# Kernel optimization log

Hardware: AMD Instinct MI355X
Metric: run time of the kernel (lower is better)

## Reference

```python
import jax, jax.numpy as jnp
import numpy as np
import math

PH, PW = 14, 14      # patch size
DH, DW = 3, 3        # DCT block size
BINS = 256


def _dct_matrix(size: int) -> np.ndarray:
    m = np.zeros((size, size), dtype=np.float32)
    for i in range(size):
        for j in range(size):
            if i == 0:
                m[i, j] = math.sqrt(1.0 / size)
            else:
                m[i, j] = math.sqrt(2.0 / size) * math.cos(math.pi * (2 * j + 1) * i / (2 * size))
    return m


def setup_inputs() -> dict:
    key = jax.random.key(0)
    x = jax.random.uniform(key, (16, 3, 448, 448), dtype=jnp.float32)
    dct_matrix = jnp.asarray(_dct_matrix(DH))
    return {"x": x, "dct_matrix": dct_matrix}


def reference(x, dct_matrix):
    B, C, H, W = x.shape
    Hp, Wp = H // PH, W // PW
    # extract non-overlapping patches -> (B, Hp, Wp, C, PH, PW)
    patches = x.reshape(B, C, Hp, PH, Wp, PW).transpose(0, 2, 4, 1, 3, 5)

    # ---- per-patch pixel-value entropy (histogram via scatter-add) ----
    N = PH * PW
    pi = jnp.clip(jnp.round(jax.lax.stop_gradient(patches) * 255.0), 0, 255).astype(jnp.int32)
    flat = pi.reshape(-1, N)                       # (P, N), P = B*Hp*Wp*C
    P = flat.shape[0]
    counts = jnp.zeros((P, BINS), jnp.float32).at[jnp.arange(P)[:, None], flat].add(1.0)
    prob = counts / N + 1e-10
    entropy = -(prob * jnp.log2(prob)).sum(-1).reshape(B, Hp, Wp, C)

    # ---- sliding 3x3 windows inside each patch (stride 1) ----
    n = PH - DH + 1                                # 12 window positions per axis
    wins = jnp.stack(
        [patches[..., di:di + n, dj:dj + n] for di in range(DH) for dj in range(DW)],
        axis=-1,
    ).reshape(B, Hp, Wp, C, n, n, DH, DW)          # last two dims = within-window offsets

    # 2D DCT: D @ block @ D^T
    dct = jnp.einsum('ij,...jk,lk->...il', dct_matrix, wins, dct_matrix)

    # ---- direction variance of normalized stds ----
    S1 = jnp.std(dct, axis=-1).mean(-1)                       # rows
    S2 = jnp.std(dct, axis=-2).mean(-1)                       # cols
    S3 = jnp.std(jnp.diagonal(dct, axis1=-2, axis2=-1), axis=-1)
    S4 = jnp.std(jnp.diagonal(jnp.flip(dct, axis=-1), axis1=-2, axis2=-1), axis=-1)
    S = (S1 + S2 + S3 + S4) / 4.0 + 1e-8
    psi = jnp.var(jnp.stack([S1 / S, S2 / S, S3 / S, S4 / S], axis=-1), axis=-1, ddof=1)
    psi_m = psi.mean(axis=(-1, -2))                           # (B, Hp, Wp, C)

    richness = psi_m * entropy
    return richness.mean(-1)                                  # (B, Hp, Wp)
```

## Files before the change

### kernel.cpp

```cpp
#include <hip/hip_runtime.h>
#include <math.h>


typedef unsigned int uint32;

__device__ __forceinline__ float fsqrt_fast(float x) { return __builtin_amdgcn_sqrtf(x); }
__device__ __forceinline__ float frcp_fast(float x)  { return __builtin_amdgcn_rcpf(x);  }
__device__ __forceinline__ float flog2_fast(float x) { return __builtin_amdgcn_logf(x);  }

__device__ __forceinline__ float std3_fast(float a, float b, float c) {
    float s = a + b + c;
    float q = fmaf(a, a, fmaf(b, b, c * c));
    float v = fmaf(q, (1.0f / 3.0f), (s * s) * (-1.0f / 9.0f));
    return fsqrt_fast(fmaxf(v, 0.0f));
}

struct RunData {
    float2 a0, a1, a2, a3, b0, b1, b2, b3, c0, c1, c2, c3;
};

__device__ __forceinline__ RunData load_run(const float* base) {
    RunData r;
    r.a0 = *reinterpret_cast<const float2*>(base + 0);
    r.a1 = *reinterpret_cast<const float2*>(base + 2);
    r.a2 = *reinterpret_cast<const float2*>(base + 4);
    r.a3 = *reinterpret_cast<const float2*>(base + 6);
    r.b0 = *reinterpret_cast<const float2*>(base + 448);
    r.b1 = *reinterpret_cast<const float2*>(base + 450);
    r.b2 = *reinterpret_cast<const float2*>(base + 452);
    r.b3 = *reinterpret_cast<const float2*>(base + 454);
    r.c0 = *reinterpret_cast<const float2*>(base + 896);
    r.c1 = *reinterpret_cast<const float2*>(base + 898);
    r.c2 = *reinterpret_cast<const float2*>(base + 900);
    r.c3 = *reinterpret_cast<const float2*>(base + 902);
    return r;
}

__device__ __forceinline__ float run_psi(const RunData& rd, float k0, float k1, float k2) {
    float r0[8] = { rd.a0.x, rd.a0.y, rd.a1.x, rd.a1.y, rd.a2.x, rd.a2.y, rd.a3.x, rd.a3.y };
    float r1[8] = { rd.b0.x, rd.b0.y, rd.b1.x, rd.b1.y, rd.b2.x, rd.b2.y, rd.b3.x, rd.b3.y };
    float r2[8] = { rd.c0.x, rd.c0.y, rd.c1.x, rd.c1.y, rd.c2.x, rd.c2.y, rd.c3.x, rd.c3.y };

    float t0[8], t1[8], t2[8];
#pragma unroll
    for (int J = 0; J < 8; ++J) {
        float s = r0[J] + r2[J];
        t0[J] = k0 * (s + r1[J]);
        t1[J] = k1 * (r0[J] - r2[J]);
        t2[J] = k2 * fmaf(-2.0f, r1[J], s);
    }

    float psi_run = 0.0f;
#pragma unroll
    for (int m = 0; m < 6; ++m) {
        float X0 = t0[m],     X1 = t1[m],     X2 = t2[m];
        float Y0 = t0[m + 1], Y1 = t1[m + 1], Y2 = t2[m + 1];
        float Z0 = t0[m + 2], Z1 = t1[m + 2], Z2 = t2[m + 2];
        float xz0 = X0 + Z0, xz1 = X1 + Z1, xz2 = X2 + Z2;
        float d00 = k0 * (xz0 + Y0), d01 = k1 * (X0 - Z0), d02 = k2 * fmaf(-2.0f, Y0, xz0);
        float d10 = k0 * (xz1 + Y1), d11 = k1 * (X1 - Z1), d12 = k2 * fmaf(-2.0f, Y1, xz1);
        float d20 = k0 * (xz2 + Y2), d21 = k1 * (X2 - Z2), d22 = k2 * fmaf(-2.0f, Y2, xz2);

        float S1 = (std3_fast(d00, d01, d02) + std3_fast(d10, d11, d12) + std3_fast(d20, d21, d22)) * (1.0f / 3.0f);
        float S2 = (std3_fast(d00, d10, d20) + std3_fast(d01, d11, d21) + std3_fast(d02, d12, d22)) * (1.0f / 3.0f);
        float S3 = std3_fast(d00, d11, d22);
        float S4 = std3_fast(d02, d11, d20);

        float sumS = (S1 + S2) + (S3 + S4);
        float sumQ = fmaf(S1, S1, fmaf(S2, S2, fmaf(S3, S3, S4 * S4)));
        float h    = fmaxf(fmaf(-0.25f * sumS, sumS, sumQ), 0.0f);
        float Sm   = fmaf(sumS, 0.25f, 1e-8f);
        float inv  = frcp_fast(Sm);
        psi_run    = fmaf(h * inv * inv, (1.0f / 3.0f), psi_run);
    }
    return psi_run;
}

#define BIN4_1CH(V, COL) { \
        _Pragma("unroll") \
        for (int e_ = 0; e_ < 4; ++e_) { \
            float val_ = (&(V).x)[e_]; \
            int bin_ = (int)rintf(val_ * 255.0f);    \
            bin_ = min(max(bin_, 0), 255); \
            int ce_ = (COL) + e_; \
            int p_  = (ce_ * 2341) >> 15;            \
            atomicAdd(&hist[p_ >> 2][bin_], 1u << ((p_ & 3) * 8)); \
        }}

__global__ __launch_bounds__(192, 8) void rich_pc_kernel(
    const float* __restrict__ x,
    const float* __restrict__ dctm,
    float* __restrict__ ws)
{
    const int bid = blockIdx.x;
    const int ch  = bid >> 11;
    const int r_  = bid & 2047;
    const int wpg = r_ & 3;
    const int hp  = (r_ >> 2) & 31;
    const int b   = r_ >> 7;
    const int tid = threadIdx.x;

    __shared__ uint32 hist[2][256];
    __shared__ float  psiPart[8][24];
    __shared__ float  entAcc[8];

    const float k0 = dctm[0];
    const float k1 = dctm[3];
    const float k2 = dctm[6];

    for (int i = tid; i < 512; i += 192) ((uint32*)hist)[i] = 0u;
    __syncthreads();

    const size_t plane = ((size_t)(b * 3 + ch) * 448 + hp * 14) * 448 + wpg * 112;

    const int pl   = tid / 24;
    const int rr   = tid - pl * 24;
    const int wi   = rr >> 1, half = rr & 1;
    const float* base = x + plane + (size_t)wi * 448 + pl * 14 + half * 6;

    int row0 = tid / 28,  col0 = (tid - row0 * 28) * 4;
    int t1_  = tid + 192;
    int row1 = t1_ / 28,  col1 = (t1_ - row1 * 28) * 4;
    const float* src0 = x + plane + (size_t)row0 * 448 + col0;
    const float* src1 = x + plane + (size_t)row1 * 448 + col1;

    RunData rd = load_run(base);
    float4 h0 = *reinterpret_cast<const float4*>(src0);
    float4 h1 = *reinterpret_cast<const float4*>(src1);

    float psi = run_psi(rd, k0, k1, k2);
    psiPart[pl][rr] = psi;

    BIN4_1CH(h0, col0)
    BIN4_1CH(h1, col1)
    if (tid < 8) {
        int colT = (20 + tid) * 4;
        const float* srcT = x + plane + (size_t)13 * 448 + colT;
        float4 hT = *reinterpret_cast<const float4*>(srcT);
        BIN4_1CH(hT, colT)
    }
    __syncthreads();

    if (tid < 64) {
        const int pcE = tid >> 3, sub = tid & 7;
        const int rowW = pcE >> 2, sh = (pcE & 3) * 8;
        float negent = 0.0f;
#pragma unroll
        for (int kk = 0; kk < 32; ++kk) {
            uint32 c = (hist[rowW][sub + 8 * kk] >> sh) & 0xffu;
            float pr = (float)c * (1.0f / 196.0f) + 1e-10f;
            negent = fmaf(pr, flog2_fast(pr), negent);
        }
#pragma unroll
        for (int off = 1; off < 8; off <<= 1) negent += __shfl_xor(negent, off, 64);
        if (sub == 0) entAcc[pcE] = -negent;
    }
    __syncthreads();

    if (tid < 8) {
        float s = 0.0f;
#pragma unroll
        for (int r = 0; r < 24; ++r) s += psiPart[tid][r];
        ws[ch * 16384 + ((b * 32 + hp) * 32 + wpg * 8 + tid)] =
            (s * (1.0f / 144.0f)) * entAcc[tid];
    }
}

__global__ __launch_bounds__(256) void combine_kernel(
    const float* __restrict__ ws, float* __restrict__ out)
{
    int i = blockIdx.x * 256 + threadIdx.x;
    out[i] = (ws[i] + ws[16384 + i] + ws[32768 + i]) * (1.0f / 3.0f);
}

__global__ __launch_bounds__(192, 6) void richness_kernel(
    const float* __restrict__ x,
    const float* __restrict__ dctm,
    float* __restrict__ out)
{
    const int bid = blockIdx.x;
    const int wpg = bid & 3;
    const int hp  = (bid >> 2) & 31;
    const int b   = bid >> 7;
    const int tid = threadIdx.x;

    __shared__ uint32 hist[6][256];
    __shared__ float  psiPart[24][24];
    __shared__ float  entAcc[24];
    __shared__ float  richAcc[24];

    const float k0 = dctm[0];
    const float k1 = dctm[3];
    const float k2 = dctm[6];

    for (int i = tid; i < 6 * 256; i += 192) ((uint32*)hist)[i] = 0u;
    __syncthreads();

#define BIN4(V, CH, COL) { \
        _Pragma("unroll") \
        for (int e_ = 0; e_ < 4; ++e_) { \
            float val_ = (&(V).x)[e_]; \
            int bin_ = (int)rintf(val_ * 255.0f); \
            bin_ = min(max(bin_, 0), 255); \
            int ce_ = (COL) + e_; \
            int p_  = (ce_ * 2341) >> 15; \
            int pc_ = (CH) * 8 + p_; \
            atomicAdd(&hist[pc_ >> 2][bin_], 1u << ((pc_ & 3) * 8)); \
        }}

    for (int t = tid; t < 1176; t += 192) {
        int ch  = t / 392;
        int rem = t - ch * 392;
        int row = rem / 28;
        int col = (rem - row * 28) * 4;
        const float* src = x + (((size_t)(b * 3 + ch) * 448 + hp * 14 + row) * 448) + wpg * 112 + col;
        float4 v = *reinterpret_cast<const float4*>(src);
        BIN4(v, ch, col)
    }

#pragma unroll
    for (int kr = 0; kr < 3; ++kr) {
        int rho = tid + 192 * kr;
        int pc  = rho / 24;
        int rr  = rho - pc * 24;
        int ch = pc >> 3, p = pc & 7;
        int wi = rr >> 1, half = rr & 1;
        const float* base = x + (((size_t)(b * 3 + ch) * 448 + hp * 14 + wi) * 448)
                              + wpg * 112 + p * 14 + half * 6;
        RunData rd = load_run(base);
        psiPart[pc][rr] = run_psi(rd, k0, k1, k2);
    }
#undef BIN4
    __syncthreads();

    {
        const int pcE = tid >> 3, sub = tid & 7;
        const int rowW = pcE >> 2, sh = (pcE & 3) * 8;
        float negent = 0.0f;
#pragma unroll
        for (int kk = 0; kk < 32; ++kk) {
            uint32 c = (hist[rowW][sub + 8 * kk] >> sh) & 0xffu;
            float pr = (float)c * (1.0f / 196.0f) + 1e-10f;
            negent = fmaf(pr, flog2_fast(pr), negent);
        }
#pragma unroll
        for (int off = 1; off < 8; off <<= 1) negent += __shfl_xor(negent, off, 64);
        if (sub == 0) entAcc[pcE] = -negent;
    }
    __syncthreads();

    if (tid < 24) {
        float s = 0.0f;
#pragma unroll
        for (int r = 0; r < 24; ++r) s += psiPart[tid][r];
        richAcc[tid] = (s * (1.0f / 144.0f)) * entAcc[tid];
    }
    __syncthreads();

    if (tid < 8) {
        float rv = (richAcc[tid] + richAcc[8 + tid] + richAcc[16 + tid]) * (1.0f / 3.0f);
        out[(b * 32 + hp) * 32 + wpg * 8 + tid] = rv;
    }
}

extern "C" void kernel_launch(void* const* d_in, const int* in_sizes, int n_in,
                              void* d_out, int out_size, void* d_ws, size_t ws_size,
                              hipStream_t stream) {
    const float* x    = (const float*)d_in[0];
    const float* dctm = (const float*)d_in[1];
    float* out        = (float*)d_out;

    if (ws_size >= 49152 * sizeof(float) && d_ws != nullptr) {
        float* ws = (float*)d_ws;
        rich_pc_kernel<<<6144, 192, 0, stream>>>(x, dctm, ws);
        combine_kernel<<<64, 256, 0, stream>>>(ws, out);
    } else {
        richness_kernel<<<2048, 192, 0, stream>>>(x, dctm, out);
    }
}
```

Baseline: 41.27 us.

## Split psi and entropy into separate kernels, fold combine into entropy pass

Replaces the per-channel fused kernel and its combine step with two kernels. A psi-only kernel needs no shared memory or block barriers: each thread processes three runs and the partial sums are reduced with wavefront shuffles. An entropy kernel builds histograms for all three channels of a patch group, then multiplies by the stored psi and averages across channels. The intent is to remove the LDS atomics and barriers from the compute-heavy psi path. The cost is that the input is read twice, once by each kernel.

```diff
diff --git a/kernel.cpp b/kernel.cpp
--- a/kernel.cpp
+++ b/kernel.cpp
@@ -76,72 +76,84 @@
     return psi_run;
 }
 
-#define BIN4_1CH(V, COL) { \
-        _Pragma("unroll") \
-        for (int e_ = 0; e_ < 4; ++e_) { \
-            float val_ = (&(V).x)[e_]; \
-            int bin_ = (int)rintf(val_ * 255.0f);    \
-            bin_ = min(max(bin_, 0), 255); \
-            int ce_ = (COL) + e_; \
-            int p_  = (ce_ * 2341) >> 15;            \
-            atomicAdd(&hist[p_ >> 2][bin_], 1u << ((p_ & 3) * 8)); \
-        }}
-
-__global__ __launch_bounds__(192, 8) void rich_pc_kernel(
+__global__ __launch_bounds__(192, 4) void psi_kernel(
     const float* __restrict__ x,
     const float* __restrict__ dctm,
     float* __restrict__ ws)
 {
     const int bid = blockIdx.x;
-    const int ch  = bid >> 11;
-    const int r_  = bid & 2047;
-    const int wpg = r_ & 3;
-    const int hp  = (r_ >> 2) & 31;
-    const int b   = r_ >> 7;
+    const int wpg = bid & 3;
+    const int hp  = (bid >> 2) & 31;
+    const int b   = bid >> 7;
     const int tid = threadIdx.x;
-
-    __shared__ uint32 hist[2][256];
-    __shared__ float  psiPart[8][24];
-    __shared__ float  entAcc[8];
 
     const float k0 = dctm[0];
     const float k1 = dctm[3];
     const float k2 = dctm[6];
 
-    for (int i = tid; i < 512; i += 192) ((uint32*)hist)[i] = 0u;
-    __syncthreads();
-
-    const size_t plane = ((size_t)(b * 3 + ch) * 448 + hp * 14) * 448 + wpg * 112;
-
-    const int pl   = tid / 24;
-    const int rr   = tid - pl * 24;
-    const int wi   = rr >> 1, half = rr & 1;
-    const float* base = x + plane + (size_t)wi * 448 + pl * 14 + half * 6;
-
-    int row0 = tid / 28,  col0 = (tid - row0 * 28) * 4;
-    int t1_  = tid + 192;
-    int row1 = t1_ / 28,  col1 = (t1_ - row1 * 28) * 4;
-    const float* src0 = x + plane + (size_t)row0 * 448 + col0;
-    const float* src1 = x + plane + (size_t)row1 * 448 + col1;
-
-    RunData rd = load_run(base);
-    float4 h0 = *reinterpret_cast<const float4*>(src0);
-    float4 h1 = *reinterpret_cast<const float4*>(src1);
-
-    float psi = run_psi(rd, k0, k1, k2);
-    psiPart[pl][rr] = psi;
-
-    BIN4_1CH(h0, col0)
-    BIN4_1CH(h1, col1)
-    if (tid < 8) {
-        int colT = (20 + tid) * 4;
-        const float* srcT = x + plane + (size_t)13 * 448 + colT;
-        float4 hT = *reinterpret_cast<const float4*>(srcT);
-        BIN4_1CH(hT, colT)
-    }
-    __syncthreads();
-
-    if (tid < 64) {
+    const int pc = tid >> 3;
+    const int s  = tid & 7;
+    const int ch = pc >> 3, pl = pc & 7;
+
+    const float* pb = x + (((size_t)(b * 3 + ch) * 448 + hp * 14) * 448) + wpg * 112 + pl * 14;
+
+    const int rj0 = s,      wi0 = rj0 >> 1, hf0 = rj0 & 1;
+    const int rj1 = s + 8,  wi1 = rj1 >> 1, hf1 = rj1 & 1;
+    const int rj2 = s + 16, wi2 = rj2 >> 1, hf2 = rj2 & 1;
+
+    RunData rd0 = load_run(pb + (size_t)wi0 * 448 + hf0 * 6);
+    RunData rd1 = load_run(pb + (size_t)wi1 * 448 + hf1 * 6);
+    float psi = run_psi(rd0, k0, k1, k2);
+    RunData rd2 = load_run(pb + (size_t)wi2 * 448 + hf2 * 6);
+    psi += run_psi(rd1, k0, k1, k2);
+    psi += run_psi(rd2, k0, k1, k2);
+
+    psi += __shfl_xor(psi, 1, 64);
+    psi += __shfl_xor(psi, 2, 64);
+    psi += __shfl_xor(psi, 4, 64);
+
+    if (s == 0)
+        ws[ch * 16384 + ((b * 32 + hp) * 32 + wpg * 8 + pl)] = psi * (1.0f / 144.0f);
+}
+
+__global__ __launch_bounds__(192, 8) void ent_kernel(
+    const float* __restrict__ x,
+    const float* __restrict__ ws,
+    float* __restrict__ out)
+{
+    const int bid = blockIdx.x;
+    const int wpg = bid & 3;
+    const int hp  = (bid >> 2) & 31;
+    const int b   = bid >> 7;
+    const int tid = threadIdx.x;
+
+    __shared__ uint32 hist[6][256];
+    __shared__ float  entAcc[24];
+
+    for (int i = tid; i < 6 * 256; i += 192) ((uint32*)hist)[i] = 0u;
+    __syncthreads();
+
+    for (int t = tid; t < 1176; t += 192) {
+        int ch  = t / 392;
+        int rem = t - ch * 392;
+        int row = rem / 28;
+        int col = (rem - row * 28) * 4;
+        const float* src = x + (((size_t)(b * 3 + ch) * 448 + hp * 14 + row) * 448) + wpg * 112 + col;
+        float4 v = *reinterpret_cast<const float4*>(src);
+#pragma unroll
+        for (int e = 0; e < 4; ++e) {
+            float val = (&v.x)[e];
+            int bin = (int)rintf(val * 255.0f);
+            bin = min(max(bin, 0), 255);
+            int ce = col + e;
+            int p  = (ce * 2341) >> 15;
+            int pc = ch * 8 + p;
+            atomicAdd(&hist[pc >> 2][bin], 1u << ((pc & 3) * 8));
+        }
+    }
+    __syncthreads();
+
+    {
         const int pcE = tid >> 3, sub = tid & 7;
         const int rowW = pcE >> 2, sh = (pcE & 3) * 8;
         float negent = 0.0f;
@@ -158,19 +170,12 @@
     __syncthreads();
 
     if (tid < 8) {
-        float s = 0.0f;
-#pragma unroll
-        for (int r = 0; r < 24; ++r) s += psiPart[tid][r];
-        ws[ch * 16384 + ((b * 32 + hp) * 32 + wpg * 8 + tid)] =
-            (s * (1.0f / 144.0f)) * entAcc[tid];
-    }
-}
-
-__global__ __launch_bounds__(256) void combine_kernel(
-    const float* __restrict__ ws, float* __restrict__ out)
-{
-    int i = blockIdx.x * 256 + threadIdx.x;
-    out[i] = (ws[i] + ws[16384 + i] + ws[32768 + i]) * (1.0f / 3.0f);
+        int pidx = (b * 32 + hp) * 32 + wpg * 8 + tid;
+        float rv = (ws[pidx]         * entAcc[tid] +
+                    ws[16384 + pidx] * entAcc[8 + tid] +
+                    ws[32768 + pidx] * entAcc[16 + tid]) * (1.0f / 3.0f);
+        out[pidx] = rv;
+    }
 }
 
 __global__ __launch_bounds__(192, 6) void richness_kernel(
@@ -196,18 +201,6 @@
     for (int i = tid; i < 6 * 256; i += 192) ((uint32*)hist)[i] = 0u;
     __syncthreads();
 
-#define BIN4(V, CH, COL) { \
-        _Pragma("unroll") \
-        for (int e_ = 0; e_ < 4; ++e_) { \
-            float val_ = (&(V).x)[e_]; \
-            int bin_ = (int)rintf(val_ * 255.0f); \
-            bin_ = min(max(bin_, 0), 255); \
-            int ce_ = (COL) + e_; \
-            int p_  = (ce_ * 2341) >> 15; \
-            int pc_ = (CH) * 8 + p_; \
-            atomicAdd(&hist[pc_ >> 2][bin_], 1u << ((pc_ & 3) * 8)); \
-        }}
-
     for (int t = tid; t < 1176; t += 192) {
         int ch  = t / 392;
         int rem = t - ch * 392;
@@ -215,7 +208,16 @@
         int col = (rem - row * 28) * 4;
         const float* src = x + (((size_t)(b * 3 + ch) * 448 + hp * 14 + row) * 448) + wpg * 112 + col;
         float4 v = *reinterpret_cast<const float4*>(src);
-        BIN4(v, ch, col)
+#pragma unroll
+        for (int e = 0; e < 4; ++e) {
+            float val = (&v.x)[e];
+            int bin = (int)rintf(val * 255.0f);
+            bin = min(max(bin, 0), 255);
+            int ce = col + e;
+            int p  = (ce * 2341) >> 15;
+            int pc = ch * 8 + p;
+            atomicAdd(&hist[pc >> 2][bin], 1u << ((pc & 3) * 8));
+        }
     }
 
 #pragma unroll
@@ -230,7 +232,6 @@
         RunData rd = load_run(base);
         psiPart[pc][rr] = run_psi(rd, k0, k1, k2);
     }
-#undef BIN4
     __syncthreads();
 
     {
@@ -272,8 +273,8 @@
 
     if (ws_size >= 49152 * sizeof(float) && d_ws != nullptr) {
         float* ws = (float*)d_ws;
-        rich_pc_kernel<<<6144, 192, 0, stream>>>(x, dctm, ws);
-        combine_kernel<<<64, 256, 0, stream>>>(ws, out);
+        psi_kernel<<<2048, 192, 0, stream>>>(x, dctm, ws);
+        ent_kernel<<<2048, 192, 0, stream>>>(x, ws, out);
     } else {
         richness_kernel<<<2048, 192, 0, stream>>>(x, dctm, out);
     }
```

Result: faster. 39.99 us (-3.1%).
